# Kernel tuning notes

Measured on AMD Instinct MI355X. Metric: run time of the kernel, lower is better.

The kernel has to match this reference:

```python
import jax, jax.numpy as jnp
import numpy as np

B, CIN, COUT, N, H, W = 8, 64, 64, 16, 32, 32

def cell_centered_grid(h, w):
    # (h, w, h, w, 4) cell-centered coords in [0,1], then mapped to [-1,1]
    dims = (h, w, h, w)
    axes = [(jnp.arange(d, dtype=jnp.float32) + 0.5) / d for d in dims]
    mesh = jnp.meshgrid(*axes, indexing='ij')
    coords = jnp.stack(mesh, axis=-1)
    return 2.0 * coords - 1.0

def setup_inputs() -> dict:
    key = jax.random.key(0)
    ks = jax.random.split(key, 9)
    v = jax.random.normal(ks[0], (B, CIN, H, W), dtype=jnp.float32)
    params = jax.random.normal(ks[1], (N, COUT, CIN), dtype=jnp.float32) / np.sqrt(N * CIN)
    # coeff_mlp: Linear(4,8) -> GELU -> Linear(8,N), torch default init
    w1 = jax.random.uniform(ks[2], (8, 4), jnp.float32, -1/np.sqrt(4), 1/np.sqrt(4))
    b1 = jax.random.uniform(ks[3], (8,), jnp.float32, -1/np.sqrt(4), 1/np.sqrt(4))
    w2 = jax.random.uniform(ks[4], (N, 8), jnp.float32, -1/np.sqrt(8), 1/np.sqrt(8))
    b2 = jax.random.uniform(ks[5], (N,), jnp.float32, -1/np.sqrt(8), 1/np.sqrt(8))
    # 1x1 conv
    cstd = 1/np.sqrt(CIN)
    conv_w = jax.random.uniform(ks[6], (COUT, CIN), jnp.float32, -cstd, cstd)
    conv_b = jax.random.uniform(ks[7], (COUT,), jnp.float32, -cstd, cstd)
    bias = jax.random.uniform(ks[8], (COUT, 1, 1), jnp.float32, -cstd, cstd)
    return {"v": v, "params": params, "w1": w1, "b1": b1, "w2": w2, "b2": b2,
            "conv_w": conv_w, "conv_b": conv_b, "bias": bias}

def reference(v, params, w1, b1, w2, b2, conv_w, conv_b, bias):
    h, w = v.shape[-2], v.shape[-1]
    coords = cell_centered_grid(h, w)                       # (h1,w1,h2,w2,4)
    hid = jax.nn.gelu(coords @ w1.T + b1, approximate=False)
    coeffs = hid @ w2.T + b2                                # (h1,w1,h2,w2,n)
    # contract coeffs with v over input spatial dims first (small intermediate)
    tmp = jnp.einsum('xyhwn,bixy->bnihw', coeffs, v)        # (B,n,i,h2,w2)
    t = jnp.einsum('bnihw,noi->bohw', tmp, params) / (h * w)
    conv = jnp.einsum('bihw,oi->bohw', v, conv_w) + conv_b[None, :, None, None]
    out = t + conv + bias[None]
    return out
```

## Files before the change

### kernel.cpp

```cpp
#include <hip/hip_runtime.h>
#include <hip/hip_bf16.h>
#include <math.h>

#define WSB_ZHW   0u
#define WSB_NODES 32768u
#define WSB_DEN   33024u
#define WSB_VSUM  33280u
#define WSB_E     35328u
#define WSB_GTAB  40960u
#define WSB_LTAB  303104u
#define WSB_QM    565248u
#define WSB_RB2   696320u
#define WSB_M1    712704u
#define WSB_WPART 843776u

__device__ inline float gelu_exact(float z) {
    return 0.5f * z * (1.0f + erff(z * 0.70710678118f));
}

__global__ __launch_bounds__(256) void prep1_kernel(const float* __restrict__ w1,
                                                    char* __restrict__ wsb) {
    float* zhw_g   = (float*)(wsb + WSB_ZHW);
    float* nodes_g = (float*)(wsb + WSB_NODES);
    float* den_g   = (float*)(wsb + WSB_DEN);
    float* Vsum    = (float*)(wsb + WSB_VSUM);
    __shared__ float zsh[8192];
    __shared__ float nodesh[64];
    int t = threadIdx.x;
    #pragma unroll
    for (int l = 0; l < 32; l++) {
        int idx = t + l * 256;
        int c = idx >> 10, hw = idx & 1023;
        float ch = 2.0f * (((hw >> 5) + 0.5f) / 32.0f) - 1.0f;
        float cw = 2.0f * (((hw & 31) + 0.5f) / 32.0f) - 1.0f;
        float val = ch * w1[c * 4 + 2] + cw * w1[c * 4 + 3];
        zsh[idx] = val;
        zhw_g[idx] = val;
    }
    Vsum[t] = 0.0f;
    Vsum[t + 256] = 0.0f;
    __syncthreads();
    if (t < 8) {
        float mn = 1e30f, mx = -1e30f;
        const float4* zp = (const float4*)&zsh[t * 1024];
        for (int j = 0; j < 256; j++) {
            float4 x = zp[j];
            mn = fminf(mn, fminf(fminf(x.x, x.y), fminf(x.z, x.w)));
            mx = fmaxf(mx, fmaxf(fmaxf(x.x, x.y), fmaxf(x.z, x.w)));
        }
        float mid = 0.5f * (mn + mx);
        float hwid = fmaxf(0.5f * (mx - mn), 1e-2f);
        #pragma unroll
        for (int r = 0; r < 8; r++) {
            float nd = mid + hwid * cosf(3.14159265358979f * (2 * r + 1) / 16.0f);
            nodesh[t * 8 + r] = nd;
            nodes_g[t * 8 + r] = nd;
        }
    }
    __syncthreads();
    if (t < 64) {
        int c = t >> 3, r = t & 7;
        float tr = nodesh[c * 8 + r];
        float d = 1.0f;
        #pragma unroll
        for (int s = 0; s < 8; s++)
            if (s != r) d *= (tr - nodesh[c * 8 + s]);
        den_g[t] = d;
    }
}

__global__ __launch_bounds__(256) void prep2_kernel(const float* __restrict__ params,
                                                    const float* __restrict__ w1,
                                                    const float* __restrict__ b1,
                                                    const float* __restrict__ w2,
                                                    const float* __restrict__ b2,
                                                    char* __restrict__ wsb) {
    const float* zhw   = (const float*)(wsb + WSB_ZHW);
    const float* nodes = (const float*)(wsb + WSB_NODES);
    const float* den   = (const float*)(wsb + WSB_DEN);
    float* Gtab = (float*)(wsb + WSB_GTAB);
    float* Ltab = (float*)(wsb + WSB_LTAB);
    float* Qm   = (float*)(wsb + WSB_QM);
    float* Rb2  = (float*)(wsb + WSB_RB2);
    int u = blockIdx.x * 256 + threadIdx.x;
    if (u < 65536) {
        int xy = u >> 6, cr = u & 63, c = cr >> 3;
        float cx = 2.0f * (((xy >> 5) + 0.5f) / 32.0f) - 1.0f;
        float cy = 2.0f * (((xy & 31) + 0.5f) / 32.0f) - 1.0f;
        float z = cx * w1[c * 4 + 0] + cy * w1[c * 4 + 1] + b1[c] + nodes[cr];
        Gtab[u] = gelu_exact(z);
    } else if (u < 131072) {
        int u2 = u - 65536;
        int cr = u2 >> 10, hw = u2 & 1023, c = cr >> 3, r = cr & 7;
        float vv = zhw[c * 1024 + hw];
        float p = 1.0f;
        #pragma unroll
        for (int s = 0; s < 8; s++)
            if (s != r) p *= (vv - nodes[c * 8 + s]);
        Ltab[u2] = p / den[cr];
    } else if (u < 163840) {
        int u2 = u - 131072;
        int c = u2 >> 12, oi = u2 & 4095;
        float s = 0.0f;
        #pragma unroll
        for (int n = 0; n < 16; n++)
            s += params[n * 4096 + oi] * w2[n * 8 + c];
        Qm[u2] = s * (1.0f / 1024.0f);
    } else {
        int oi = u - 163840;
        float s = 0.0f;
        #pragma unroll
        for (int n = 0; n < 16; n++)
            s += params[n * 4096 + oi] * b2[n];
        Rb2[oi] = s * (1.0f / 1024.0f);
    }
}

__global__ __launch_bounds__(256) void wgemm_kernel(const float* __restrict__ v,
                                                    char* __restrict__ wsb) {
    const float* Gtab = (const float*)(wsb + WSB_GTAB);
    float* Wpart = (float*)(wsb + WSB_WPART);
    float* Vsum  = (float*)(wsb + WSB_VSUM);
    __shared__ float Vs[16][68];
    __shared__ float Gs[64][64];
    int t = threadIdx.x;
    int bi0 = blockIdx.x * 16, xy0 = blockIdx.y * 64;
    {
        int r = t >> 4, c4 = t & 15;
        *(float4*)&Vs[r][c4 * 4] = *(const float4*)(v + (bi0 + r) * 1024 + xy0 + c4 * 4);
    }
    #pragma unroll
    for (int l = 0; l < 4; l++) {
        int e = t + l * 256;
        int xy = e >> 4, q = e & 15;
        *(float4*)&Gs[xy][q * 4] = *(const float4*)(Gtab + (size_t)(xy0 + xy) * 64 + q * 4);
    }
    __syncthreads();
    int bl = t >> 4, crq = t & 15;
    float4 acc = make_float4(0.f, 0.f, 0.f, 0.f);
    float vs = 0.0f;
    #pragma unroll 8
    for (int xy = 0; xy < 64; xy++) {
        float a = Vs[bl][xy];
        float4 g = *(const float4*)&Gs[xy][crq * 4];
        acc.x += a * g.x; acc.y += a * g.y; acc.z += a * g.z; acc.w += a * g.w;
        vs += a;
    }
    *(float4*)(Wpart + (size_t)blockIdx.y * 32768 + (bi0 + bl) * 64 + crq * 4) = acc;
    if (crq == 0) atomicAdd(&Vsum[bi0 + bl], vs);
}

__global__ __launch_bounds__(256) void m1_kernel(const float* __restrict__ conv_b,
                                                 const float* __restrict__ bias,
                                                 char* __restrict__ wsb) {
    const float* Qm    = (const float*)(wsb + WSB_QM);
    const float* Wpart = (const float*)(wsb + WSB_WPART);
    const float* Rb2   = (const float*)(wsb + WSB_RB2);
    const float* Vsum  = (const float*)(wsb + WSB_VSUM);
    float* M1 = (float*)(wsb + WSB_M1);
    float* E  = (float*)(wsb + WSB_E);
    __shared__ float Qsh[64 * 64];
    __shared__ float Wsht[8][64];
    int c = blockIdx.x, b = blockIdx.y;
    int t = threadIdx.x;
    #pragma unroll
    for (int l = 0; l < 16; l++) {
        int e = t + l * 256;
        Qsh[e] = Qm[c * 4096 + e];
    }
    #pragma unroll
    for (int l = 0; l < 2; l++) {
        int e = t + l * 256;
        int i = e >> 3, r = e & 7;
        float s = 0.0f;
        #pragma unroll
        for (int ks = 0; ks < 16; ks++)
            s += Wpart[(size_t)ks * 32768 + (b * 64 + i) * 64 + c * 8 + r];
        Wsht[r][i] = s;
    }
    __syncthreads();
    #pragma unroll
    for (int l = 0; l < 2; l++) {
        int m = t + l * 256;
        int o = m >> 3, r = m & 7;
        float acc = 0.0f;
        #pragma unroll
        for (int i4 = 0; i4 < 16; i4++) {
            float4 q = *(const float4*)&Qsh[o * 64 + i4 * 4];
            float4 w = *(const float4*)&Wsht[r][i4 * 4];
            acc += q.x * w.x + q.y * w.y + q.z * w.z + q.w * w.w;
        }
        M1[b * 4096 + o * 64 + c * 8 + r] = acc;
    }
    if (c == 0 && t < 64) {
        float s = conv_b[t] + bias[t];
        for (int i = 0; i < 64; i++)
            s += Rb2[t * 64 + i] * Vsum[b * 64 + i];
        E[b * 64 + t] = s;
    }
}

__global__ __launch_bounds__(256) void final_kernel(const float* __restrict__ v,
                                                    const float* __restrict__ conv_w,
                                                    float* __restrict__ out,
                                                    char* __restrict__ wsb) {
    const float* Ltab = (const float*)(wsb + WSB_LTAB);
    const float* M1   = (const float*)(wsb + WSB_M1);
    const float* E    = (const float*)(wsb + WSB_E);
    __shared__ float Ct[128][36];
    __shared__ float Ys[128][64];
    int t = threadIdx.x;
    int hw0 = blockIdx.x * 64, o0 = blockIdx.y * 32, b = blockIdx.z;
    #pragma unroll
    for (int l = 0; l < 16; l++) {
        int e = t + l * 256;
        int ol = e >> 7, k = e & 127;
        float val = (k < 64) ? M1[b * 4096 + (o0 + ol) * 64 + k]
                             : conv_w[(o0 + ol) * 64 + (k - 64)];
        Ct[k][ol] = val;
    }
    #pragma unroll
    for (int l = 0; l < 8; l++) {
        int f = t + l * 256;
        int k = f >> 4, q = f & 15;
        const float* src = (k < 64) ? (Ltab + (size_t)k * 1024)
                                    : (v + (size_t)b * 65536 + (k - 64) * 1024);
        *(float4*)&Ys[k][q * 4] = *(const float4*)(src + hw0 + q * 4);
    }
    __syncthreads();
    int ty = t >> 5, tx = t & 31;
    float acc[4][2];
    #pragma unroll
    for (int m = 0; m < 4; m++) {
        float e = E[b * 64 + o0 + ty * 4 + m];
        acc[m][0] = e; acc[m][1] = e;
    }
    #pragma unroll 4
    for (int k = 0; k < 128; k++) {
        float4 cq = *(const float4*)&Ct[k][ty * 4];
        float2 y = *(const float2*)&Ys[k][tx * 2];
        acc[0][0] += cq.x * y.x; acc[0][1] += cq.x * y.y;
        acc[1][0] += cq.y * y.x; acc[1][1] += cq.y * y.y;
        acc[2][0] += cq.z * y.x; acc[2][1] += cq.z * y.y;
        acc[3][0] += cq.w * y.x; acc[3][1] += cq.w * y.y;
    }
    #pragma unroll
    for (int m = 0; m < 4; m++) {
        float2 r = make_float2(acc[m][0], acc[m][1]);
        *(float2*)(out + (size_t)b * 65536 + (o0 + ty * 4 + m) * 1024 + hw0 + tx * 2) = r;
    }
}

extern "C" void kernel_launch(void* const* d_in, const int* in_sizes, int n_in,
                              void* d_out, int out_size, void* d_ws, size_t ws_size,
                              hipStream_t stream) {
    const float* v      = (const float*)d_in[0];
    const float* params = (const float*)d_in[1];
    const float* w1     = (const float*)d_in[2];
    const float* b1     = (const float*)d_in[3];
    const float* w2     = (const float*)d_in[4];
    const float* b2     = (const float*)d_in[5];
    const float* conv_w = (const float*)d_in[6];
    const float* conv_b = (const float*)d_in[7];
    const float* bias   = (const float*)d_in[8];
    float* out = (float*)d_out;
    char* wsb  = (char*)d_ws;

    prep1_kernel<<<1, 256, 0, stream>>>(w1, wsb);
    prep2_kernel<<<656, 256, 0, stream>>>(params, w1, b1, w2, b2, wsb);
    wgemm_kernel<<<dim3(32, 16), 256, 0, stream>>>(v, wsb);
    m1_kernel<<<dim3(8, 8), 256, 0, stream>>>(conv_b, bias, wsb);
    final_kernel<<<dim3(16, 2, 8), 256, 0, stream>>>(v, conv_w, out, wsb);
}
```

Before: 100.9 us.

## Fold node setup into prep kernel and fuse M1 reduction into final kernel

Drops the single-block prep1 kernel by computing Chebyshev nodes in closed form from w1 (the min/max of the linear grid map is |w2|+|w3| times 31/32, and the mid is zero). Merges m1_kernel into final_kernel, so each block reduces Wpart, forms its slice of M1 and the bias term E in shared memory before the GEMM. Five launches become three, and a serial one-block kernel leaves the critical path. The cost is redundant work: each of the 16 hw-blocks per (o-tile, b) repeats the Wpart reduction and the Q·W product.

```diff
diff --git a/kernel.cpp b/kernel.cpp
--- a/kernel.cpp
+++ b/kernel.cpp
@@ -2,102 +2,61 @@
 #include <hip/hip_bf16.h>
 #include <math.h>
 
-#define WSB_ZHW   0u
-#define WSB_NODES 32768u
-#define WSB_DEN   33024u
-#define WSB_VSUM  33280u
-#define WSB_E     35328u
-#define WSB_GTAB  40960u
-#define WSB_LTAB  303104u
-#define WSB_QM    565248u
-#define WSB_RB2   696320u
-#define WSB_M1    712704u
-#define WSB_WPART 843776u
+#define WSB_VSUM  0u
+#define WSB_GTAB  4096u
+#define WSB_LTAB  266240u
+#define WSB_QM    528384u
+#define WSB_RB2   659456u
+#define WSB_WPART 675840u
+
+#define COS8_INIT {0.98078528f, 0.83146961f, 0.55557023f, 0.19509032f, \
+                  -0.19509032f, -0.55557023f, -0.83146961f, -0.98078528f}
 
 __device__ inline float gelu_exact(float z) {
     return 0.5f * z * (1.0f + erff(z * 0.70710678118f));
 }
 
-__global__ __launch_bounds__(256) void prep1_kernel(const float* __restrict__ w1,
-                                                    char* __restrict__ wsb) {
-    float* zhw_g   = (float*)(wsb + WSB_ZHW);
-    float* nodes_g = (float*)(wsb + WSB_NODES);
-    float* den_g   = (float*)(wsb + WSB_DEN);
-    float* Vsum    = (float*)(wsb + WSB_VSUM);
-    __shared__ float zsh[8192];
-    __shared__ float nodesh[64];
-    int t = threadIdx.x;
-    #pragma unroll
-    for (int l = 0; l < 32; l++) {
-        int idx = t + l * 256;
-        int c = idx >> 10, hw = idx & 1023;
-        float ch = 2.0f * (((hw >> 5) + 0.5f) / 32.0f) - 1.0f;
-        float cw = 2.0f * (((hw & 31) + 0.5f) / 32.0f) - 1.0f;
-        float val = ch * w1[c * 4 + 2] + cw * w1[c * 4 + 3];
-        zsh[idx] = val;
-        zhw_g[idx] = val;
-    }
-    Vsum[t] = 0.0f;
-    Vsum[t + 256] = 0.0f;
-    __syncthreads();
-    if (t < 8) {
-        float mn = 1e30f, mx = -1e30f;
-        const float4* zp = (const float4*)&zsh[t * 1024];
-        for (int j = 0; j < 256; j++) {
-            float4 x = zp[j];
-            mn = fminf(mn, fminf(fminf(x.x, x.y), fminf(x.z, x.w)));
-            mx = fmaxf(mx, fmaxf(fmaxf(x.x, x.y), fmaxf(x.z, x.w)));
-        }
-        float mid = 0.5f * (mn + mx);
-        float hwid = fmaxf(0.5f * (mx - mn), 1e-2f);
-        #pragma unroll
-        for (int r = 0; r < 8; r++) {
-            float nd = mid + hwid * cosf(3.14159265358979f * (2 * r + 1) / 16.0f);
-            nodesh[t * 8 + r] = nd;
-            nodes_g[t * 8 + r] = nd;
-        }
-    }
-    __syncthreads();
-    if (t < 64) {
-        int c = t >> 3, r = t & 7;
-        float tr = nodesh[c * 8 + r];
-        float d = 1.0f;
-        #pragma unroll
-        for (int s = 0; s < 8; s++)
-            if (s != r) d *= (tr - nodesh[c * 8 + s]);
-        den_g[t] = d;
-    }
-}
-
-__global__ __launch_bounds__(256) void prep2_kernel(const float* __restrict__ params,
-                                                    const float* __restrict__ w1,
-                                                    const float* __restrict__ b1,
-                                                    const float* __restrict__ w2,
-                                                    const float* __restrict__ b2,
-                                                    char* __restrict__ wsb) {
-    const float* zhw   = (const float*)(wsb + WSB_ZHW);
-    const float* nodes = (const float*)(wsb + WSB_NODES);
-    const float* den   = (const float*)(wsb + WSB_DEN);
+__device__ inline float cheb_hwid(const float* w1, int c) {
+    return fmaxf((fabsf(w1[c * 4 + 2]) + fabsf(w1[c * 4 + 3])) * (31.0f / 32.0f), 1e-2f);
+}
+
+__global__ __launch_bounds__(256) void prep_kernel(const float* __restrict__ params,
+                                                   const float* __restrict__ w1,
+                                                   const float* __restrict__ b1,
+                                                   const float* __restrict__ w2,
+                                                   const float* __restrict__ b2,
+                                                   char* __restrict__ wsb) {
+    const float COS8[8] = COS8_INIT;
     float* Gtab = (float*)(wsb + WSB_GTAB);
     float* Ltab = (float*)(wsb + WSB_LTAB);
     float* Qm   = (float*)(wsb + WSB_QM);
     float* Rb2  = (float*)(wsb + WSB_RB2);
+    float* Vsum = (float*)(wsb + WSB_VSUM);
     int u = blockIdx.x * 256 + threadIdx.x;
     if (u < 65536) {
-        int xy = u >> 6, cr = u & 63, c = cr >> 3;
+        int xy = u >> 6, cr = u & 63, c = cr >> 3, r = cr & 7;
         float cx = 2.0f * (((xy >> 5) + 0.5f) / 32.0f) - 1.0f;
         float cy = 2.0f * (((xy & 31) + 0.5f) / 32.0f) - 1.0f;
-        float z = cx * w1[c * 4 + 0] + cy * w1[c * 4 + 1] + b1[c] + nodes[cr];
+        float z = cx * w1[c * 4 + 0] + cy * w1[c * 4 + 1] + b1[c]
+                + cheb_hwid(w1, c) * COS8[r];
         Gtab[u] = gelu_exact(z);
     } else if (u < 131072) {
         int u2 = u - 65536;
         int cr = u2 >> 10, hw = u2 & 1023, c = cr >> 3, r = cr & 7;
-        float vv = zhw[c * 1024 + hw];
-        float p = 1.0f;
+        float hwid = cheb_hwid(w1, c);
+        float ch = 2.0f * (((hw >> 5) + 0.5f) / 32.0f) - 1.0f;
+        float cw = 2.0f * (((hw & 31) + 0.5f) / 32.0f) - 1.0f;
+        float vv = ch * w1[c * 4 + 2] + cw * w1[c * 4 + 3];
+        float tr = hwid * COS8[r];
+        float p = 1.0f, d = 1.0f;
         #pragma unroll
         for (int s = 0; s < 8; s++)
-            if (s != r) p *= (vv - nodes[c * 8 + s]);
-        Ltab[u2] = p / den[cr];
+            if (s != r) {
+                float ts = hwid * COS8[s];
+                p *= (vv - ts);
+                d *= (tr - ts);
+            }
+        Ltab[u2] = p / d;
     } else if (u < 163840) {
         int u2 = u - 131072;
         int c = u2 >> 12, oi = u2 & 4095;
@@ -106,13 +65,15 @@
         for (int n = 0; n < 16; n++)
             s += params[n * 4096 + oi] * w2[n * 8 + c];
         Qm[u2] = s * (1.0f / 1024.0f);
-    } else {
+    } else if (u < 167936) {
         int oi = u - 163840;
         float s = 0.0f;
         #pragma unroll
         for (int n = 0; n < 16; n++)
             s += params[n * 4096 + oi] * b2[n];
         Rb2[oi] = s * (1.0f / 1024.0f);
+    } else {
+        Vsum[u - 167936] = 0.0f;
     }
 }
 
@@ -150,95 +111,103 @@
     if (crq == 0) atomicAdd(&Vsum[bi0 + bl], vs);
 }
 
-__global__ __launch_bounds__(256) void m1_kernel(const float* __restrict__ conv_b,
-                                                 const float* __restrict__ bias,
-                                                 char* __restrict__ wsb) {
+__global__ __launch_bounds__(256) void final_kernel(const float* __restrict__ v,
+                                                    const float* __restrict__ conv_w,
+                                                    const float* __restrict__ conv_b,
+                                                    const float* __restrict__ bias,
+                                                    float* __restrict__ out,
+                                                    char* __restrict__ wsb) {
+    const float* Ltab  = (const float*)(wsb + WSB_LTAB);
     const float* Qm    = (const float*)(wsb + WSB_QM);
-    const float* Wpart = (const float*)(wsb + WSB_WPART);
     const float* Rb2   = (const float*)(wsb + WSB_RB2);
     const float* Vsum  = (const float*)(wsb + WSB_VSUM);
-    float* M1 = (float*)(wsb + WSB_M1);
-    float* E  = (float*)(wsb + WSB_E);
-    __shared__ float Qsh[64 * 64];
-    __shared__ float Wsht[8][64];
-    int c = blockIdx.x, b = blockIdx.y;
-    int t = threadIdx.x;
-    #pragma unroll
-    for (int l = 0; l < 16; l++) {
-        int e = t + l * 256;
-        Qsh[e] = Qm[c * 4096 + e];
-    }
-    #pragma unroll
-    for (int l = 0; l < 2; l++) {
-        int e = t + l * 256;
-        int i = e >> 3, r = e & 7;
-        float s = 0.0f;
-        #pragma unroll
-        for (int ks = 0; ks < 16; ks++)
-            s += Wpart[(size_t)ks * 32768 + (b * 64 + i) * 64 + c * 8 + r];
-        Wsht[r][i] = s;
-    }
-    __syncthreads();
-    #pragma unroll
-    for (int l = 0; l < 2; l++) {
-        int m = t + l * 256;
-        int o = m >> 3, r = m & 7;
-        float acc = 0.0f;
-        #pragma unroll
-        for (int i4 = 0; i4 < 16; i4++) {
-            float4 q = *(const float4*)&Qsh[o * 64 + i4 * 4];
-            float4 w = *(const float4*)&Wsht[r][i4 * 4];
-            acc += q.x * w.x + q.y * w.y + q.z * w.z + q.w * w.w;
-        }
-        M1[b * 4096 + o * 64 + c * 8 + r] = acc;
-    }
-    if (c == 0 && t < 64) {
-        float s = conv_b[t] + bias[t];
-        for (int i = 0; i < 64; i++)
-            s += Rb2[t * 64 + i] * Vsum[b * 64 + i];
-        E[b * 64 + t] = s;
-    }
-}
-
-__global__ __launch_bounds__(256) void final_kernel(const float* __restrict__ v,
-                                                    const float* __restrict__ conv_w,
-                                                    float* __restrict__ out,
-                                                    char* __restrict__ wsb) {
-    const float* Ltab = (const float*)(wsb + WSB_LTAB);
-    const float* M1   = (const float*)(wsb + WSB_M1);
-    const float* E    = (const float*)(wsb + WSB_E);
-    __shared__ float Ct[128][36];
-    __shared__ float Ys[128][64];
+    const float* Wpart = (const float*)(wsb + WSB_WPART);
+    __shared__ float smem[128 * 36 + 128 * 64];
+    __shared__ float Esh[32];
+    float* Ct = smem;
+    float* Ys = smem + 128 * 36;
+    float* Wsum = Ys;
     int t = threadIdx.x;
     int hw0 = blockIdx.x * 64, o0 = blockIdx.y * 32, b = blockIdx.z;
-    #pragma unroll
-    for (int l = 0; l < 16; l++) {
+
+    {
+        int e0 = t * 16;
+        float4 a0 = {0,0,0,0}, a1 = {0,0,0,0}, a2 = {0,0,0,0}, a3 = {0,0,0,0};
+        const float* wp = Wpart + b * 4096 + e0;
+        #pragma unroll
+        for (int ks = 0; ks < 16; ks++) {
+            const float4* p = (const float4*)(wp + (size_t)ks * 32768);
+            float4 x0 = p[0], x1 = p[1], x2 = p[2], x3 = p[3];
+            a0.x += x0.x; a0.y += x0.y; a0.z += x0.z; a0.w += x0.w;
+            a1.x += x1.x; a1.y += x1.y; a1.z += x1.z; a1.w += x1.w;
+            a2.x += x2.x; a2.y += x2.y; a2.z += x2.z; a2.w += x2.w;
+            a3.x += x3.x; a3.y += x3.y; a3.z += x3.z; a3.w += x3.w;
+        }
+        *(float4*)&Wsum[e0]      = a0;
+        *(float4*)&Wsum[e0 + 4]  = a1;
+        *(float4*)&Wsum[e0 + 8]  = a2;
+        *(float4*)&Wsum[e0 + 12] = a3;
+    }
+    #pragma unroll
+    for (int l = 0; l < 8; l++) {
         int e = t + l * 256;
-        int ol = e >> 7, k = e & 127;
-        float val = (k < 64) ? M1[b * 4096 + (o0 + ol) * 64 + k]
-                             : conv_w[(o0 + ol) * 64 + (k - 64)];
-        Ct[k][ol] = val;
-    }
-    #pragma unroll
-    for (int l = 0; l < 8; l++) {
+        int kk = e >> 5, ol = e & 31;
+        Ct[(64 + kk) * 36 + ol] = conv_w[(o0 + ol) * 64 + kk];
+    }
+    #pragma unroll
+    for (int l = 0; l < 4; l++) {
         int f = t + l * 256;
         int k = f >> 4, q = f & 15;
-        const float* src = (k < 64) ? (Ltab + (size_t)k * 1024)
-                                    : (v + (size_t)b * 65536 + (k - 64) * 1024);
-        *(float4*)&Ys[k][q * 4] = *(const float4*)(src + hw0 + q * 4);
-    }
-    __syncthreads();
+        *(float4*)&Ys[(64 + k) * 64 + q * 4] =
+            *(const float4*)(v + (size_t)b * 65536 + k * 1024 + hw0 + q * 4);
+    }
+    __syncthreads();
+
+    {
+        int ol = t >> 3, c = t & 7;
+        float a[8] = {};
+        const float* qrow = Qm + c * 4096 + (o0 + ol) * 64;
+        for (int i = 0; i < 64; i++) {
+            float q = qrow[i];
+            float4 w0 = *(const float4*)&Wsum[i * 64 + c * 8];
+            float4 w1v = *(const float4*)&Wsum[i * 64 + c * 8 + 4];
+            a[0] += q * w0.x; a[1] += q * w0.y; a[2] += q * w0.z; a[3] += q * w0.w;
+            a[4] += q * w1v.x; a[5] += q * w1v.y; a[6] += q * w1v.z; a[7] += q * w1v.w;
+        }
+        #pragma unroll
+        for (int r = 0; r < 8; r++)
+            Ct[(c * 8 + r) * 36 + ol] = a[r];
+    }
+    if (t < 32) {
+        int o = o0 + t;
+        float s = conv_b[o] + bias[o];
+        const float* rr = Rb2 + o * 64;
+        const float* vs = Vsum + b * 64;
+        for (int i = 0; i < 64; i++) s += rr[i] * vs[i];
+        Esh[t] = s;
+    }
+    __syncthreads();
+
+    #pragma unroll
+    for (int l = 0; l < 4; l++) {
+        int f = t + l * 256;
+        int k = f >> 4, q = f & 15;
+        *(float4*)&Ys[k * 64 + q * 4] =
+            *(const float4*)(Ltab + (size_t)k * 1024 + hw0 + q * 4);
+    }
+    __syncthreads();
+
     int ty = t >> 5, tx = t & 31;
     float acc[4][2];
     #pragma unroll
     for (int m = 0; m < 4; m++) {
-        float e = E[b * 64 + o0 + ty * 4 + m];
+        float e = Esh[ty * 4 + m];
         acc[m][0] = e; acc[m][1] = e;
     }
     #pragma unroll 4
     for (int k = 0; k < 128; k++) {
-        float4 cq = *(const float4*)&Ct[k][ty * 4];
-        float2 y = *(const float2*)&Ys[k][tx * 2];
+        float4 cq = *(const float4*)&Ct[k * 36 + ty * 4];
+        float2 y = *(const float2*)&Ys[k * 64 + tx * 2];
         acc[0][0] += cq.x * y.x; acc[0][1] += cq.x * y.y;
         acc[1][0] += cq.y * y.x; acc[1][1] += cq.y * y.y;
         acc[2][0] += cq.z * y.x; acc[2][1] += cq.z * y.y;
@@ -266,9 +235,7 @@
     float* out = (float*)d_out;
     char* wsb  = (char*)d_ws;
 
-    prep1_kernel<<<1, 256, 0, stream>>>(w1, wsb);
-    prep2_kernel<<<656, 256, 0, stream>>>(params, w1, b1, w2, b2, wsb);
+    prep_kernel<<<658, 256, 0, stream>>>(params, w1, b1, w2, b2, wsb);
     wgemm_kernel<<<dim3(32, 16), 256, 0, stream>>>(v, wsb);
-    m1_kernel<<<dim3(8, 8), 256, 0, stream>>>(conv_b, bias, wsb);
-    final_kernel<<<dim3(16, 2, 8), 256, 0, stream>>>(v, conv_w, out, wsb);
-}
+    final_kernel<<<dim3(16, 2, 8), 256, 0, stream>>>(v, conv_w, conv_b, bias, out, wsb);
+}
```

Result: faster. 94.55 us (-6.3%).
